# Kernel tuning notes

Measured on AMD Instinct MI355X. Metric: run time of the kernel, lower is better.

Reference implementation:

```python
import jax, jax.numpy as jnp
import numpy as np

EPS = 1e-5
HEADS, DK, DV = 8, 32, 64
SCALE = DK ** -0.5

def _bn(x, gamma, beta, mean, var):
    # eval-mode BatchNorm1d over channel dim of [b, c, n]
    inv = gamma / jnp.sqrt(var + EPS)
    return (x - mean[None, :, None]) * inv[None, :, None] + beta[None, :, None]

def setup_inputs() -> dict:
    key = jax.random.key(0)
    ks = jax.random.split(key, 24)
    dim, n, dim_out = 256, 1024, 256
    idk, idv = DK * HEADS, DV * HEADS
    def bn_params(k, c):
        k1, k2, k3, k4 = jax.random.split(k, 4)
        return (jax.random.normal(k1, (c,)) * 0.1 + 1.0,   # gamma
                jax.random.normal(k2, (c,)) * 0.1,          # beta
                jax.random.normal(k3, (c,)) * 0.1,          # running mean
                jax.random.uniform(k4, (c,)) * 0.5 + 0.5)   # running var > 0
    q_g, q_b, q_m, q_v = bn_params(ks[1], idk)
    k_g, k_b, k_m, k_v = bn_params(ks[2], idk)
    v_g, v_b, v_m, v_v = bn_params(ks[3], idv)
    o_g, o_b, o_m, o_v = bn_params(ks[4], dim_out)
    return {
        'x': jax.random.normal(ks[0], (8, dim, n), dtype=jnp.float32),
        'Wq': jax.random.normal(ks[5], (idk, dim)) * (dim ** -0.5),
        'Wk': jax.random.normal(ks[6], (idk, dim)) * (dim ** -0.5),
        'Wv': jax.random.normal(ks[7], (idv, dim)) * (dim ** -0.5),
        'Wo': jax.random.normal(ks[8], (dim_out, idv)) * (idv ** -0.5),
        'bo': jax.random.normal(ks[9], (dim_out,)) * 0.02,
        'pos_emb': jax.random.normal(ks[10], (n, HEADS)) * 0.02,
        'q_gamma': q_g, 'q_beta': q_b, 'q_mean': q_m, 'q_var': q_v,
        'k_gamma': k_g, 'k_beta': k_b, 'k_mean': k_m, 'k_var': k_v,
        'v_gamma': v_g, 'v_beta': v_b, 'v_mean': v_m, 'v_var': v_v,
        'o_gamma': o_g, 'o_beta': o_b, 'o_mean': o_m, 'o_var': o_v,
    }

def reference(x, Wq, Wk, Wv, Wo, bo, pos_emb,
              q_gamma, q_beta, q_mean, q_var,
              k_gamma, k_beta, k_mean, k_var,
              v_gamma, v_beta, v_mean, v_var,
              o_gamma, o_beta, o_mean, o_var):
    b, _, n = x.shape
    # 1x1 conv == channel matmul, then BN
    q = _bn(jnp.einsum('bcn,oc->bon', x, Wq), q_gamma, q_beta, q_mean, q_var)
    k = _bn(jnp.einsum('bcn,oc->bon', x, Wk), k_gamma, k_beta, k_mean, k_var)
    v = _bn(jnp.einsum('bcn,oc->bon', x, Wv), v_gamma, v_beta, v_mean, v_var)
    # b (h d) n -> b h n d
    q = q.reshape(b, HEADS, DK, n).transpose(0, 1, 3, 2)
    k = k.reshape(b, HEADS, DK, n).transpose(0, 1, 3, 2)
    v = v.reshape(b, HEADS, DV, n).transpose(0, 1, 3, 2)
    dots = jnp.einsum('bhid,bhjd->bhij', q, k) * SCALE
    # relative-position bias: emb[|i-j|] -> [n, n, h] -> [1, h, n, n]
    rel = jnp.abs(jnp.arange(n)[:, None] - jnp.arange(n)[None, :])
    bias = pos_emb[rel].transpose(2, 0, 1)[None]
    dots = dots + bias / SCALE
    attn = jax.nn.softmax(dots, axis=-1)
    out = jnp.einsum('bhij,bhjd->bhid', attn, v)
    # b h n d -> b (h d) n
    out = out.transpose(0, 1, 3, 2).reshape(b, HEADS * DV, n)
    out = jax.nn.gelu(out, approximate=False)
    out = jnp.einsum('bcn,oc->bon', out, Wo) + bo[None, :, None]
    return _bn(out, o_gamma, o_beta, o_mean, o_var)
```

## Files before the change

### kernel.cpp

```cpp
#include <hip/hip_runtime.h>
#include <hip/hip_bf16.h>

#define HEADS 8
#define DK 32
#define DV 64
#define DIM 256
#define NCTX 1024
#define NB 8
#define IDK 256
#define IDV 512
#define SCALE 0.17677669529663687f
#define INV_SCALE 5.656854249492381f
#define LOG2E 1.4426950408889634f
#define BN_EPS 1e-5f
#define THR 11.5416f

typedef __bf16 bf16x8 __attribute__((ext_vector_type(8)));
typedef __bf16 bf16x4 __attribute__((ext_vector_type(4)));
typedef float f32x4 __attribute__((ext_vector_type(4)));
typedef float f32x16 __attribute__((ext_vector_type(16)));

static __device__ __forceinline__ unsigned short bfbits(float v) {
  __bf16 b = (__bf16)v;
  return __builtin_bit_cast(unsigned short, b);
}

__global__ __launch_bounds__(256) void k_prep_trans(
    const float* __restrict__ x,
    const float* __restrict__ Wq, const float* __restrict__ Wk,
    const float* __restrict__ Wv, const float* __restrict__ Wo,
    const float* __restrict__ bo, const float* __restrict__ pe,
    const float* __restrict__ qg, const float* __restrict__ qb,
    const float* __restrict__ qm, const float* __restrict__ qv,
    const float* __restrict__ kg, const float* __restrict__ kb,
    const float* __restrict__ km, const float* __restrict__ kv,
    const float* __restrict__ vg, const float* __restrict__ vb,
    const float* __restrict__ vm, const float* __restrict__ vv,
    const float* __restrict__ og, const float* __restrict__ ob,
    const float* __restrict__ om, const float* __restrict__ ov,
    __bf16* __restrict__ xT, __bf16* __restrict__ WB, float* __restrict__ BB,
    uint2* __restrict__ Tq4g) {
  int bid = blockIdx.x;
  if (bid < 1605) {
    int idx = bid * 256 + threadIdx.x;
    if (idx < 65536) {
      int o = idx >> 8;
      WB[idx] = (__bf16)(Wq[idx] * (qg[o] * rsqrtf(qv[o] + BN_EPS) * SCALE * LOG2E));
    } else if (idx < 131072) {
      int i = idx - 65536, o = i >> 8;
      WB[idx] = (__bf16)(Wk[i] * (kg[o] * rsqrtf(kv[o] + BN_EPS)));
    } else if (idx < 262144) {
      int i = idx - 131072, o = i >> 8;
      WB[idx] = (__bf16)(Wv[i] * (vg[o] * rsqrtf(vv[o] + BN_EPS)));
    } else if (idx < 393216) {
      int i = idx - 262144, o = i >> 9;
      WB[idx] = (__bf16)(Wo[i] * (og[o] * rsqrtf(ov[o] + BN_EPS)));
    } else if (idx < 394496) {
      int i = idx - 393216;
      if (i < 256) {
        float sc = qg[i] * rsqrtf(qv[i] + BN_EPS);
        BB[i] = (qb[i] - qm[i] * sc) * SCALE * LOG2E;
      } else if (i < 512) {
        int o = i - 256;
        float sc = kg[o] * rsqrtf(kv[o] + BN_EPS);
        BB[i] = kb[o] - km[o] * sc;
      } else if (i < 1024) {
        int o = i - 512;
        float sc = vg[o] * rsqrtf(vv[o] + BN_EPS);
        BB[i] = vb[o] - vm[o] * sc;
      } else {
        int o = i - 1024;
        float sc = og[o] * rsqrtf(ov[o] + BN_EPS);
        BB[i] = (bo[o] - om[o]) * sc + ob[o];
      }
    } else {
      int i = idx - 394496;
      int h = i >> 11, t = i & 2047;
      unsigned short us[4];
#pragma unroll
      for (int rr = 0; rr < 4; ++rr) {
        int d = t - rr - 1023; d = d < 0 ? -d : d; d = d > 1023 ? 1023 : d;
        us[rr] = bfbits(pe[(size_t)d * HEADS + h] * INV_SCALE * LOG2E);
      }
      uint2 e;
      e.x = (unsigned)us[0] | ((unsigned)us[1] << 16);
      e.y = (unsigned)us[2] | ((unsigned)us[3] << 16);
      Tq4g[((size_t)h << 11) + t] = e;
    }
  } else {
    __shared__ float t[64][65];
    int tb = bid - 1605;
    int b = tb >> 6, c0 = ((tb >> 4) & 3) * 64, n0 = (tb & 15) * 64;
    int col = threadIdx.x & 63, rb = threadIdx.x >> 6;
    const float* xp = x + ((size_t)b * DIM + c0) * NCTX + n0;
#pragma unroll
    for (int r = 0; r < 16; ++r) {
      int row = rb + 4 * r;
      t[row][col] = xp[(size_t)row * NCTX + col];
    }
    __syncthreads();
    __bf16* op = xT + ((size_t)b * NCTX + n0) * DIM + c0;
#pragma unroll
    for (int r = 0; r < 16; ++r) {
      int i = rb + 4 * r;
      op[(size_t)i * DIM + col] = (__bf16)t[col][i];
    }
  }
}

__global__ __launch_bounds__(256, 2) void k_gemm_qkv(
    const __bf16* __restrict__ Xsrc, const __bf16* __restrict__ Wsrc,
    const float* __restrict__ Bias, __bf16* __restrict__ Qws,
    __bf16* __restrict__ Kws, __bf16* __restrict__ Vws) {
  int bx = blockIdx.x, by = blockIdx.y;
  int mode = by < 2 ? 0 : (by < 4 ? 1 : 2);
  int tid = threadIdx.x, wave = tid >> 6, lane = tid & 63;
  int wm = wave >> 1, wn = wave & 1;
  int l16 = lane & 15, g = (lane >> 4) & 3, g4 = g * 4;
  int R0 = bx * 128;

  __shared__ __align__(16) char XTl[16384];
  __shared__ __align__(16) char WTl[16384];

  int sr = tid >> 1, sh = tid & 1;
  const __bf16* xg = Xsrc + (size_t)(R0 + sr) * DIM + sh * 32;
  const __bf16* wg = Wsrc + (size_t)(by * 128 + sr) * DIM + sh * 32;
  int wbase = sr * 128;
  int gsw[4];
#pragma unroll
  for (int q = 0; q < 4; ++q) gsw[q] = ((sh * 4 + q) ^ (sr & 7)) * 16;

  bf16x8 sx[4], sw[4];
#pragma unroll
  for (int q = 0; q < 4; ++q) {
    sx[q] = *reinterpret_cast<const bf16x8*>(xg + q * 8);
    sw[q] = *reinterpret_cast<const bf16x8*>(wg + q * 8);
  }

  f32x4 acc[4][4] = {};
  const char* Abase = (mode <= 1) ? WTl : XTl;
  const char* Bbase = (mode <= 1) ? XTl : WTl;

  for (int st = 0; st < 4; ++st) {
    __syncthreads();
#pragma unroll
    for (int q = 0; q < 4; ++q) {
      *reinterpret_cast<bf16x8*>(XTl + wbase + gsw[q]) = sx[q];
      *reinterpret_cast<bf16x8*>(WTl + wbase + gsw[q]) = sw[q];
    }
    __syncthreads();
    if (st + 1 < 4) {
      const __bf16* xn = xg + (st + 1) * 64;
      const __bf16* wn_ = wg + (st + 1) * 64;
#pragma unroll
      for (int q = 0; q < 4; ++q) {
        sx[q] = *reinterpret_cast<const bf16x8*>(xn + q * 8);
        sw[q] = *reinterpret_cast<const bf16x8*>(wn_ + q * 8);
      }
    }
#pragma unroll
    for (int kc = 0; kc < 2; ++kc) {
      bf16x8 af[4], bf[4];
#pragma unroll
      for (int t = 0; t < 4; ++t) {
        int ra = wm * 64 + t * 16 + l16;
        af[t] = *reinterpret_cast<const bf16x8*>(
            Abase + ra * 128 + (((kc * 4 + g) ^ (ra & 7)) * 16));
        int rb = wn * 64 + t * 16 + l16;
        bf[t] = *reinterpret_cast<const bf16x8*>(
            Bbase + rb * 128 + (((kc * 4 + g) ^ (rb & 7)) * 16));
      }
      __builtin_amdgcn_s_setprio(1);
#pragma unroll
      for (int mt = 0; mt < 4; ++mt)
#pragma unroll
        for (int nt = 0; nt < 4; ++nt)
          acc[mt][nt] = __builtin_amdgcn_mfma_f32_16x16x32_bf16(
              af[mt], bf[nt], acc[mt][nt], 0, 0, 0);
      __builtin_amdgcn_s_setprio(0);
    }
  }

  if (mode <= 1) {
    __bf16* OWS = (mode == 0) ? Qws : Kws;
    const float* bb = Bias + (mode == 0 ? 0 : 256);
    int oq0 = by * 128 - (mode == 1 ? 256 : 0) + wm * 64;
#pragma unroll
    for (int mt = 0; mt < 4; ++mt) {
      int oq = oq0 + mt * 16 + g4;
      float4 b4 = *reinterpret_cast<const float4*>(&bb[oq]);
      int h = oq >> 5, d0 = oq & 31;
#pragma unroll
      for (int nt = 0; nt < 4; ++nt) {
        int i = R0 + wn * 64 + nt * 16 + l16;
        int b = i >> 10, n = i & 1023;
        bf16x4 pk;
        pk[0] = (__bf16)(acc[mt][nt][0] + b4.x);
        pk[1] = (__bf16)(acc[mt][nt][1] + b4.y);
        pk[2] = (__bf16)(acc[mt][nt][2] + b4.z);
        pk[3] = (__bf16)(acc[mt][nt][3] + b4.w);
        *reinterpret_cast<bf16x4*>(
            &OWS[(((size_t)b * HEADS + h) * NCTX + n) * DK + d0]) = pk;
      }
    }
  } else {
#pragma unroll
    for (int nt = 0; nt < 4; ++nt) {
      int vo = (by - 4) * 128 + wn * 64 + nt * 16 + l16;
      float bia = Bias[512 + vo];
#pragma unroll
      for (int mt = 0; mt < 4; ++mt) {
        int i0 = R0 + wm * 64 + mt * 16 + g4;
        int b = i0 >> 10, n = i0 & 1023;
        bf16x4 pk;
#pragma unroll
        for (int rr = 0; rr < 4; ++rr) pk[rr] = (__bf16)(acc[mt][nt][rr] + bia);
        *reinterpret_cast<bf16x4*>(&Vws[((size_t)b * IDV + vo) * NCTX + n]) = pk;
      }
    }
  }
}

__global__ __launch_bounds__(256, 4) void k_gemm_out(
    const __bf16* __restrict__ G, const __bf16* __restrict__ WoB,
    const float* __restrict__ bo2, float* __restrict__ out) {
  int bx = blockIdx.x, by = blockIdx.y;
  int tid = threadIdx.x, wave = tid >> 6, lane = tid & 63;
  int wm = wave >> 1, wn = wave & 1;
  int l16 = lane & 15, g = (lane >> 4) & 3, g4 = g * 4;
  int R0 = bx * 64;

  __shared__ __align__(16) char XTl[8192];
  __shared__ __align__(16) char WTl[8192];

  int sr = tid >> 2, sq = tid & 3;
  const __bf16* xg = G + (size_t)(R0 + sr) * IDV + sq * 16;
  const __bf16* wg = WoB + (size_t)(by * 64 + sr) * IDV + sq * 16;
  int sbase = sr * 128;
  int gswq[2];
#pragma unroll
  for (int q = 0; q < 2; ++q) gswq[q] = ((sq * 2 + q) ^ (sr & 7)) * 16;

  bf16x8 sx[2], sw[2];
#pragma unroll
  for (int q = 0; q < 2; ++q) {
    sx[q] = *reinterpret_cast<const bf16x8*>(xg + q * 8);
    sw[q] = *reinterpret_cast<const bf16x8*>(wg + q * 8);
  }

  f32x4 acc[2][2] = {};

  for (int st = 0; st < 8; ++st) {
    __syncthreads();
#pragma unroll
    for (int q = 0; q < 2; ++q) {
      *reinterpret_cast<bf16x8*>(XTl + sbase + gswq[q]) = sx[q];
      *reinterpret_cast<bf16x8*>(WTl + sbase + gswq[q]) = sw[q];
    }
    __syncthreads();
    if (st + 1 < 8) {
      const __bf16* xn = xg + (st + 1) * 64;
      const __bf16* wn_ = wg + (st + 1) * 64;
#pragma unroll
      for (int q = 0; q < 2; ++q) {
        sx[q] = *reinterpret_cast<const bf16x8*>(xn + q * 8);
        sw[q] = *reinterpret_cast<const bf16x8*>(wn_ + q * 8);
      }
    }
#pragma unroll
    for (int kc = 0; kc < 2; ++kc) {
      bf16x8 af[2], bf[2];
#pragma unroll
      for (int t = 0; t < 2; ++t) {
        int ra = wm * 32 + t * 16 + l16;
        af[t] = *reinterpret_cast<const bf16x8*>(
            XTl + ra * 128 + (((kc * 4 + g) ^ (ra & 7)) * 16));
        int rb = wn * 32 + t * 16 + l16;
        bf[t] = *reinterpret_cast<const bf16x8*>(
            WTl + rb * 128 + (((kc * 4 + g) ^ (rb & 7)) * 16));
      }
      __builtin_amdgcn_s_setprio(1);
#pragma unroll
      for (int mt = 0; mt < 2; ++mt)
#pragma unroll
        for (int nt = 0; nt < 2; ++nt)
          acc[mt][nt] = __builtin_amdgcn_mfma_f32_16x16x32_bf16(
              af[mt], bf[nt], acc[mt][nt], 0, 0, 0);
      __builtin_amdgcn_s_setprio(0);
    }
  }
#pragma unroll
  for (int nt = 0; nt < 2; ++nt) {
    int o = by * 64 + wn * 32 + nt * 16 + l16;
    float bia = bo2[o];
#pragma unroll
    for (int mt = 0; mt < 2; ++mt) {
      int i0 = R0 + wm * 32 + mt * 16 + g4;
      int b = i0 >> 10, n = i0 & 1023;
      float4 st;
      st.x = acc[mt][nt][0] + bia;
      st.y = acc[mt][nt][1] + bia;
      st.z = acc[mt][nt][2] + bia;
      st.w = acc[mt][nt][3] + bia;
      *reinterpret_cast<float4*>(&out[((size_t)b * DIM + o) * NCTX + n]) = st;
    }
  }
}

__global__ __launch_bounds__(256, 4) void k_attn(
    const __bf16* __restrict__ Qws, const __bf16* __restrict__ Kws,
    const __bf16* __restrict__ Vws, const uint2* __restrict__ Tq4g,
    __bf16* __restrict__ G) {
  int flat = blockIdx.x;
  int swz = (flat & 7) * 64 + (flat >> 3);
  int iblk = swz & 7, bh = swz >> 3;
  int b = bh >> 3, h = bh & 7;
  int tid = threadIdx.x, wave = tid >> 6, lane = tid & 63;
  int l31 = lane & 31, hi = lane >> 5;

  __shared__ __align__(16) __bf16 Klds[2][64][40];
  __shared__ __align__(16) __bf16 Vlds[2][64 * 64];
  __shared__ __align__(16) uint2 TqL[1152];

  int i0b = iblk * 128;
  {
    const uint4* tg4 = reinterpret_cast<const uint4*>(Tq4g + ((size_t)h << 11) + i0b);
    uint4* tl4 = reinterpret_cast<uint4*>(TqL);
    for (int c = tid; c < 576; c += 256) tl4[c] = tg4[c];
  }

  int i0w = i0b + wave * 32;
  int irow = i0w + l31;
  const __bf16* qbase = Qws + (size_t)bh * NCTX * DK;
  const __bf16* kbase = Kws + (size_t)bh * NCTX * DK;
  const __bf16* vbase = Vws + ((size_t)b * IDV + h * DV) * NCTX;
  bf16x8 qf0 = *reinterpret_cast<const bf16x8*>(qbase + (size_t)irow * DK + 8 * hi);
  bf16x8 qf1 = *reinterpret_cast<const bf16x8*>(qbase + (size_t)irow * DK + 16 + 8 * hi);

  int r_ = tid >> 2, sk = tid & 3;
  const __bf16* kgp = kbase + (size_t)r_ * DK + 8 * sk;
  const __bf16* vgp = vbase + (size_t)r_ * NCTX + 8 * sk;
  int ko = r_ * 40 + 8 * sk;
  int vo0 = r_ * 64 + 8 * (sk ^ (r_ & 7));
  int vo1 = r_ * 64 + 8 * ((sk + 4) ^ (r_ & 7));

  bf16x8 rk = *reinterpret_cast<const bf16x8*>(kgp);
  bf16x8 rv0 = *reinterpret_cast<const bf16x8*>(vgp);
  bf16x8 rv1 = *reinterpret_cast<const bf16x8*>(vgp + 32);
  *reinterpret_cast<bf16x8*>(&Klds[0][0][0] + ko) = rk;
  *reinterpret_cast<bf16x8*>(&Vlds[0][0] + vo0) = rv0;
  *reinterpret_cast<bf16x8*>(&Vlds[0][0] + vo1) = rv1;

  f32x16 acc0 = {}, acc1 = {};
  float m = -1e30f, s = 0.0f;
  int kxb = wave * 32 + l31 + 1023 - 4 * hi;
  const bf16x4* Tqp = reinterpret_cast<const bf16x4*>(TqL);

  __syncthreads();

  for (int it = 0; it < 16; ++it) {
    int cur = it & 1, nxt = cur ^ 1;
    int j0 = it * 64;
    int jn = (j0 + 64) & (NCTX - 1);
    rk = *reinterpret_cast<const bf16x8*>(kgp + (size_t)jn * DK);
    rv0 = *reinterpret_cast<const bf16x8*>(vgp + jn);
    rv1 = *reinterpret_cast<const bf16x8*>(vgp + jn + 32);

    float sv[32];
#pragma unroll
    for (int jg = 0; jg < 2; ++jg) {
      bf16x8 kf0 = *reinterpret_cast<const bf16x8*>(&Klds[cur][32 * jg + l31][8 * hi]);
      bf16x8 kf1 = *reinterpret_cast<const bf16x8*>(&Klds[cur][32 * jg + l31][16 + 8 * hi]);
      f32x16 S = {};
      __builtin_amdgcn_s_setprio(1);
      S = __builtin_amdgcn_mfma_f32_32x32x16_bf16(kf0, qf0, S, 0, 0, 0);
      S = __builtin_amdgcn_mfma_f32_32x32x16_bf16(kf1, qf1, S, 0, 0, 0);
      __builtin_amdgcn_s_setprio(0);
      int kb_ = kxb - j0 - 32 * jg;
#pragma unroll
      for (int q = 0; q < 4; ++q) {
        bf16x4 q4 = Tqp[kb_ - 8 * q];
#pragma unroll
        for (int rr = 0; rr < 4; ++rr)
          sv[jg * 16 + q * 4 + rr] = S[q * 4 + rr] + (float)q4[rr];
      }
    }
    float pmax = sv[0];
#pragma unroll
    for (int k = 1; k < 32; ++k) pmax = fmaxf(pmax, sv[k]);
    if (__any(pmax > m + THR)) {
      float mx = fmaxf(pmax, __shfl_xor(pmax, 32));
      float mnew = fmaxf(m, mx);
      float corr = __builtin_amdgcn_exp2f(m - mnew);
      s *= corr; m = mnew;
#pragma unroll
      for (int r = 0; r < 16; ++r) {
        float cv = __shfl(corr, (r & 3) + 8 * (r >> 2) + 4 * hi);
        acc0[r] *= cv; acc1[r] *= cv;
      }
    }
#pragma unroll
    for (int k = 0; k < 32; ++k) sv[k] = __builtin_amdgcn_exp2f(sv[k] - m);
    float ps = 0.0f;
#pragma unroll
    for (int k = 0; k < 32; ++k) ps += sv[k];
    s += ps;
#pragma unroll
    for (int jg = 0; jg < 2; ++jg) {
#pragma unroll
      for (int u = 0; u < 2; ++u) {
        int base = jg * 16 + 8 * u;
        unsigned we0, we1, wo0, wo1;
        asm("v_cvt_pk_bf16_f32 %0, %1, %2" : "=v"(we0) : "v"(sv[base + 0]), "v"(sv[base + 1]));
        asm("v_cvt_pk_bf16_f32 %0, %1, %2" : "=v"(we1) : "v"(sv[base + 2]), "v"(sv[base + 3]));
        asm("v_cvt_pk_bf16_f32 %0, %1, %2" : "=v"(wo0) : "v"(sv[base + 4]), "v"(sv[base + 5]));
        asm("v_cvt_pk_bf16_f32 %0, %1, %2" : "=v"(wo1) : "v"(sv[base + 6]), "v"(sv[base + 7]));
        asm volatile("v_permlane32_swap_b32 %0, %1" : "+v"(we0), "+v"(wo0));
        asm volatile("v_permlane32_swap_b32 %0, %1" : "+v"(we1), "+v"(wo1));
        uint4 pw = {we0, we1, wo0, wo1};
        bf16x8 pfrag = *reinterpret_cast<bf16x8*>(&pw);
        int sl = 2 * (jg * 2 + u) + hi;
        bf16x8 vf0 = *reinterpret_cast<const bf16x8*>(
            &Vlds[cur][0] + l31 * 64 + 8 * (sl ^ (l31 & 7)));
        bf16x8 vf1 = *reinterpret_cast<const bf16x8*>(
            &Vlds[cur][0] + (32 + l31) * 64 + 8 * (sl ^ (l31 & 7)));
        __builtin_amdgcn_s_setprio(1);
        acc0 = __builtin_amdgcn_mfma_f32_32x32x16_bf16(pfrag, vf0, acc0, 0, 0, 0);
        acc1 = __builtin_amdgcn_mfma_f32_32x32x16_bf16(pfrag, vf1, acc1, 0, 0, 0);
        __builtin_amdgcn_s_setprio(0);
      }
    }
    *reinterpret_cast<bf16x8*>(&Klds[nxt][0][0] + ko) = rk;
    *reinterpret_cast<bf16x8*>(&Vlds[nxt][0] + vo0) = rv0;
    *reinterpret_cast<bf16x8*>(&Vlds[nxt][0] + vo1) = rv1;
    __syncthreads();
  }
  float srow = s + __shfl_xor(s, 32);
  float inv = 1.0f / srow;
  __bf16* gbase = G + (size_t)b * NCTX * IDV + h * DV + l31;
#pragma unroll
  for (int r = 0; r < 16; ++r) {
    int il = (r & 3) + 8 * (r >> 2) + 4 * hi;
    float iv = __shfl(inv, il);
    float v0 = acc0[r] * iv, v1 = acc1[r] * iv;
    float g0 = 0.5f * v0 * (1.0f + erff(v0 * 0.70710678118654752f));
    float g1 = 0.5f * v1 * (1.0f + erff(v1 * 0.70710678118654752f));
    gbase[(size_t)(i0w + il) * IDV] = (__bf16)g0;
    gbase[(size_t)(i0w + il) * IDV + 32] = (__bf16)g1;
  }
}

extern "C" void kernel_launch(void* const* d_in, const int* in_sizes, int n_in,
                              void* d_out, int out_size, void* d_ws, size_t ws_size,
                              hipStream_t stream) {
  const float* x  = (const float*)d_in[0];
  const float* Wq = (const float*)d_in[1];
  const float* Wk = (const float*)d_in[2];
  const float* Wv = (const float*)d_in[3];
  const float* Wo = (const float*)d_in[4];
  const float* bo = (const float*)d_in[5];
  const float* pe = (const float*)d_in[6];
  const float* qg = (const float*)d_in[7];
  const float* qb = (const float*)d_in[8];
  const float* qm = (const float*)d_in[9];
  const float* qv = (const float*)d_in[10];
  const float* kg = (const float*)d_in[11];
  const float* kb = (const float*)d_in[12];
  const float* km = (const float*)d_in[13];
  const float* kv = (const float*)d_in[14];
  const float* vg = (const float*)d_in[15];
  const float* vb = (const float*)d_in[16];
  const float* vm = (const float*)d_in[17];
  const float* vv = (const float*)d_in[18];
  const float* og = (const float*)d_in[19];
  const float* ob = (const float*)d_in[20];
  const float* om = (const float*)d_in[21];
  const float* ov = (const float*)d_in[22];

  char* ws = (char*)d_ws;
  __bf16* xT = (__bf16*)(ws);
  __bf16* Q  = (__bf16*)(ws + (4ull << 20));
  __bf16* K  = (__bf16*)(ws + (8ull << 20));
  __bf16* V  = (__bf16*)(ws + (12ull << 20));
  __bf16* G  = (__bf16*)(ws + (20ull << 20));
  __bf16* WB = (__bf16*)(ws + (28ull << 20));
  float*  BB = (float*)(ws + (28ull << 20) + (768ull << 10));
  uint2*  Tq = (uint2*)(ws + (29ull << 20));
  float* out = (float*)d_out;

  k_prep_trans<<<dim3(2117), 256, 0, stream>>>(
      x, Wq, Wk, Wv, Wo, bo, pe, qg, qb, qm, qv, kg, kb, km, kv,
      vg, vb, vm, vv, og, ob, om, ov, xT, WB, BB, Tq);
  k_gemm_qkv<<<dim3(64, 8), 256, 0, stream>>>(xT, WB, BB, Q, K, V);
  k_attn<<<dim3(512), 256, 0, stream>>>(Q, K, V, Tq, G);
  k_gemm_out<<<dim3(128, 4), 256, 0, stream>>>(G, WB + 262144, BB + 1024, out);
}
```

Baseline: 56.78 us.

## Deepen attention K/V prefetch to two tiles ahead with register ping-pong

The attention loop is unrolled by two so K/V global loads are issued two tiles ahead into alternating register sets (A/B), while the LDS double buffer stays. This gives global loads more time in flight before their LDS store. It costs more registers, so the launch bound drops from 4 to 3 blocks per SM, which reduces occupancy.

```diff
diff --git a/kernel.cpp b/kernel.cpp
--- a/kernel.cpp
+++ b/kernel.cpp
@@ -307,7 +307,7 @@
   }
 }
 
-__global__ __launch_bounds__(256, 4) void k_attn(
+__global__ __launch_bounds__(256, 3) void k_attn(
     const __bf16* __restrict__ Qws, const __bf16* __restrict__ Kws,
     const __bf16* __restrict__ Vws, const uint2* __restrict__ Tq4g,
     __bf16* __restrict__ G) {
@@ -344,97 +344,127 @@
   int vo0 = r_ * 64 + 8 * (sk ^ (r_ & 7));
   int vo1 = r_ * 64 + 8 * ((sk + 4) ^ (r_ & 7));
 
-  bf16x8 rk = *reinterpret_cast<const bf16x8*>(kgp);
-  bf16x8 rv0 = *reinterpret_cast<const bf16x8*>(vgp);
-  bf16x8 rv1 = *reinterpret_cast<const bf16x8*>(vgp + 32);
-  *reinterpret_cast<bf16x8*>(&Klds[0][0][0] + ko) = rk;
-  *reinterpret_cast<bf16x8*>(&Vlds[0][0] + vo0) = rv0;
-  *reinterpret_cast<bf16x8*>(&Vlds[0][0] + vo1) = rv1;
-
   f32x16 acc0 = {}, acc1 = {};
   float m = -1e30f, s = 0.0f;
   int kxb = wave * 32 + l31 + 1023 - 4 * hi;
   const bf16x4* Tqp = reinterpret_cast<const bf16x4*>(TqL);
 
+  {
+    bf16x8 t0k = *reinterpret_cast<const bf16x8*>(kgp);
+    bf16x8 t0v0 = *reinterpret_cast<const bf16x8*>(vgp);
+    bf16x8 t0v1 = *reinterpret_cast<const bf16x8*>(vgp + 32);
+    *reinterpret_cast<bf16x8*>(&Klds[0][0][0] + ko) = t0k;
+    *reinterpret_cast<bf16x8*>(&Vlds[0][0] + vo0) = t0v0;
+    *reinterpret_cast<bf16x8*>(&Vlds[0][0] + vo1) = t0v1;
+  }
+  bf16x8 kA = *reinterpret_cast<const bf16x8*>(kgp + (size_t)64 * DK);
+  bf16x8 v0A = *reinterpret_cast<const bf16x8*>(vgp + 64);
+  bf16x8 v1A = *reinterpret_cast<const bf16x8*>(vgp + 96);
+  bf16x8 kB, v0B, v1B;
+
   __syncthreads();
 
-  for (int it = 0; it < 16; ++it) {
-    int cur = it & 1, nxt = cur ^ 1;
-    int j0 = it * 64;
-    int jn = (j0 + 64) & (NCTX - 1);
-    rk = *reinterpret_cast<const bf16x8*>(kgp + (size_t)jn * DK);
-    rv0 = *reinterpret_cast<const bf16x8*>(vgp + jn);
-    rv1 = *reinterpret_cast<const bf16x8*>(vgp + jn + 32);
-
-    float sv[32];
-#pragma unroll
-    for (int jg = 0; jg < 2; ++jg) {
-      bf16x8 kf0 = *reinterpret_cast<const bf16x8*>(&Klds[cur][32 * jg + l31][8 * hi]);
-      bf16x8 kf1 = *reinterpret_cast<const bf16x8*>(&Klds[cur][32 * jg + l31][16 + 8 * hi]);
-      f32x16 S = {};
-      __builtin_amdgcn_s_setprio(1);
-      S = __builtin_amdgcn_mfma_f32_32x32x16_bf16(kf0, qf0, S, 0, 0, 0);
-      S = __builtin_amdgcn_mfma_f32_32x32x16_bf16(kf1, qf1, S, 0, 0, 0);
-      __builtin_amdgcn_s_setprio(0);
-      int kb_ = kxb - j0 - 32 * jg;
-#pragma unroll
-      for (int q = 0; q < 4; ++q) {
-        bf16x4 q4 = Tqp[kb_ - 8 * q];
-#pragma unroll
-        for (int rr = 0; rr < 4; ++rr)
-          sv[jg * 16 + q * 4 + rr] = S[q * 4 + rr] + (float)q4[rr];
-      }
-    }
-    float pmax = sv[0];
-#pragma unroll
-    for (int k = 1; k < 32; ++k) pmax = fmaxf(pmax, sv[k]);
-    if (__any(pmax > m + THR)) {
-      float mx = fmaxf(pmax, __shfl_xor(pmax, 32));
-      float mnew = fmaxf(m, mx);
-      float corr = __builtin_amdgcn_exp2f(m - mnew);
-      s *= corr; m = mnew;
-#pragma unroll
-      for (int r = 0; r < 16; ++r) {
-        float cv = __shfl(corr, (r & 3) + 8 * (r >> 2) + 4 * hi);
-        acc0[r] *= cv; acc1[r] *= cv;
-      }
-    }
-#pragma unroll
-    for (int k = 0; k < 32; ++k) sv[k] = __builtin_amdgcn_exp2f(sv[k] - m);
-    float ps = 0.0f;
-#pragma unroll
-    for (int k = 0; k < 32; ++k) ps += sv[k];
-    s += ps;
-#pragma unroll
-    for (int jg = 0; jg < 2; ++jg) {
-#pragma unroll
-      for (int u = 0; u < 2; ++u) {
-        int base = jg * 16 + 8 * u;
-        unsigned we0, we1, wo0, wo1;
-        asm("v_cvt_pk_bf16_f32 %0, %1, %2" : "=v"(we0) : "v"(sv[base + 0]), "v"(sv[base + 1]));
-        asm("v_cvt_pk_bf16_f32 %0, %1, %2" : "=v"(we1) : "v"(sv[base + 2]), "v"(sv[base + 3]));
-        asm("v_cvt_pk_bf16_f32 %0, %1, %2" : "=v"(wo0) : "v"(sv[base + 4]), "v"(sv[base + 5]));
-        asm("v_cvt_pk_bf16_f32 %0, %1, %2" : "=v"(wo1) : "v"(sv[base + 6]), "v"(sv[base + 7]));
-        asm volatile("v_permlane32_swap_b32 %0, %1" : "+v"(we0), "+v"(wo0));
-        asm volatile("v_permlane32_swap_b32 %0, %1" : "+v"(we1), "+v"(wo1));
-        uint4 pw = {we0, we1, wo0, wo1};
-        bf16x8 pfrag = *reinterpret_cast<bf16x8*>(&pw);
-        int sl = 2 * (jg * 2 + u) + hi;
-        bf16x8 vf0 = *reinterpret_cast<const bf16x8*>(
-            &Vlds[cur][0] + l31 * 64 + 8 * (sl ^ (l31 & 7)));
-        bf16x8 vf1 = *reinterpret_cast<const bf16x8*>(
-            &Vlds[cur][0] + (32 + l31) * 64 + 8 * (sl ^ (l31 & 7)));
-        __builtin_amdgcn_s_setprio(1);
-        acc0 = __builtin_amdgcn_mfma_f32_32x32x16_bf16(pfrag, vf0, acc0, 0, 0, 0);
-        acc1 = __builtin_amdgcn_mfma_f32_32x32x16_bf16(pfrag, vf1, acc1, 0, 0, 0);
-        __builtin_amdgcn_s_setprio(0);
-      }
-    }
-    *reinterpret_cast<bf16x8*>(&Klds[nxt][0][0] + ko) = rk;
-    *reinterpret_cast<bf16x8*>(&Vlds[nxt][0] + vo0) = rv0;
-    *reinterpret_cast<bf16x8*>(&Vlds[nxt][0] + vo1) = rv1;
-    __syncthreads();
-  }
+#define ATTN_STEP(CUR, J0)                                                        \
+  {                                                                               \
+    float sv[32];                                                                 \
+    _Pragma("unroll")                                                             \
+    for (int jg = 0; jg < 2; ++jg) {                                              \
+      bf16x8 kf0 = *reinterpret_cast<const bf16x8*>(                              \
+          &Klds[CUR][32 * jg + l31][8 * hi]);                                     \
+      bf16x8 kf1 = *reinterpret_cast<const bf16x8*>(                              \
+          &Klds[CUR][32 * jg + l31][16 + 8 * hi]);                                \
+      f32x16 S = {};                                                              \
+      __builtin_amdgcn_s_setprio(1);                                              \
+      S = __builtin_amdgcn_mfma_f32_32x32x16_bf16(kf0, qf0, S, 0, 0, 0);          \
+      S = __builtin_amdgcn_mfma_f32_32x32x16_bf16(kf1, qf1, S, 0, 0, 0);          \
+      __builtin_amdgcn_s_setprio(0);                                              \
+      int kb_ = kxb - (J0) - 32 * jg;                                             \
+      _Pragma("unroll")                                                           \
+      for (int q = 0; q < 4; ++q) {                                               \
+        bf16x4 q4 = Tqp[kb_ - 8 * q];                                             \
+        _Pragma("unroll")                                                         \
+        for (int rr = 0; rr < 4; ++rr)                                            \
+          sv[jg * 16 + q * 4 + rr] = S[q * 4 + rr] + (float)q4[rr];               \
+      }                                                                           \
+    }                                                                             \
+    float pmax = sv[0];                                                           \
+    _Pragma("unroll")                                                             \
+    for (int k = 1; k < 32; ++k) pmax = fmaxf(pmax, sv[k]);                       \
+    if (__any(pmax > m + THR)) {                                                  \
+      float mx = fmaxf(pmax, __shfl_xor(pmax, 32));                               \
+      float mnew = fmaxf(m, mx);                                                  \
+      float corr = __builtin_amdgcn_exp2f(m - mnew);                              \
+      s *= corr; m = mnew;                                                        \
+      _Pragma("unroll")                                                           \
+      for (int r = 0; r < 16; ++r) {                                              \
+        float cv = __shfl(corr, (r & 3) + 8 * (r >> 2) + 4 * hi);                 \
+        acc0[r] *= cv; acc1[r] *= cv;                                             \
+      }                                                                           \
+    }                                                                             \
+    _Pragma("unroll")                                                             \
+    for (int k = 0; k < 32; ++k) sv[k] = __builtin_amdgcn_exp2f(sv[k] - m);       \
+    float ps = 0.0f;                                                              \
+    _Pragma("unroll")                                                             \
+    for (int k = 0; k < 32; ++k) ps += sv[k];                                     \
+    s += ps;                                                                      \
+    _Pragma("unroll")                                                             \
+    for (int jg = 0; jg < 2; ++jg) {                                              \
+      _Pragma("unroll")                                                           \
+      for (int u = 0; u < 2; ++u) {                                               \
+        int base = jg * 16 + 8 * u;                                               \
+        unsigned we0, we1, wo0, wo1;                                              \
+        asm("v_cvt_pk_bf16_f32 %0, %1, %2"                                        \
+            : "=v"(we0) : "v"(sv[base + 0]), "v"(sv[base + 1]));                  \
+        asm("v_cvt_pk_bf16_f32 %0, %1, %2"                                        \
+            : "=v"(we1) : "v"(sv[base + 2]), "v"(sv[base + 3]));                  \
+        asm("v_cvt_pk_bf16_f32 %0, %1, %2"                                        \
+            : "=v"(wo0) : "v"(sv[base + 4]), "v"(sv[base + 5]));                  \
+        asm("v_cvt_pk_bf16_f32 %0, %1, %2"                                        \
+            : "=v"(wo1) : "v"(sv[base + 6]), "v"(sv[base + 7]));                  \
+        asm volatile("v_permlane32_swap_b32 %0, %1" : "+v"(we0), "+v"(wo0));      \
+        asm volatile("v_permlane32_swap_b32 %0, %1" : "+v"(we1), "+v"(wo1));      \
+        uint4 pw = {we0, we1, wo0, wo1};                                          \
+        bf16x8 pfrag = *reinterpret_cast<bf16x8*>(&pw);                           \
+        int sl = 2 * (jg * 2 + u) + hi;                                           \
+        bf16x8 vf0 = *reinterpret_cast<const bf16x8*>(                            \
+            &Vlds[CUR][0] + l31 * 64 + 8 * (sl ^ (l31 & 7)));                     \
+        bf16x8 vf1 = *reinterpret_cast<const bf16x8*>(                            \
+            &Vlds[CUR][0] + (32 + l31) * 64 + 8 * (sl ^ (l31 & 7)));              \
+        __builtin_amdgcn_s_setprio(1);                                            \
+        acc0 = __builtin_amdgcn_mfma_f32_32x32x16_bf16(pfrag, vf0, acc0, 0,0,0);  \
+        acc1 = __builtin_amdgcn_mfma_f32_32x32x16_bf16(pfrag, vf1, acc1, 0,0,0);  \
+        __builtin_amdgcn_s_setprio(0);                                            \
+      }                                                                           \
+    }                                                                             \
+  }
+
+  for (int it2 = 0; it2 < 8; ++it2) {
+    int t = it2 * 2;
+    {
+      int jn = ((t + 2) * 64) & (NCTX - 1);
+      kB = *reinterpret_cast<const bf16x8*>(kgp + (size_t)jn * DK);
+      v0B = *reinterpret_cast<const bf16x8*>(vgp + jn);
+      v1B = *reinterpret_cast<const bf16x8*>(vgp + jn + 32);
+      ATTN_STEP(0, t * 64);
+      *reinterpret_cast<bf16x8*>(&Klds[1][0][0] + ko) = kA;
+      *reinterpret_cast<bf16x8*>(&Vlds[1][0] + vo0) = v0A;
+      *reinterpret_cast<bf16x8*>(&Vlds[1][0] + vo1) = v1A;
+      __syncthreads();
+    }
+    {
+      int jn = ((t + 3) * 64) & (NCTX - 1);
+      kA = *reinterpret_cast<const bf16x8*>(kgp + (size_t)jn * DK);
+      v0A = *reinterpret_cast<const bf16x8*>(vgp + jn);
+      v1A = *reinterpret_cast<const bf16x8*>(vgp + jn + 32);
+      ATTN_STEP(1, (t + 1) * 64);
+      *reinterpret_cast<bf16x8*>(&Klds[0][0][0] + ko) = kB;
+      *reinterpret_cast<bf16x8*>(&Vlds[0][0] + vo0) = v0B;
+      *reinterpret_cast<bf16x8*>(&Vlds[0][0] + vo1) = v1B;
+      __syncthreads();
+    }
+  }
+#undef ATTN_STEP
+
   float srow = s + __shfl_xor(s, 32);
   float inv = 1.0f / srow;
   __bf16* gbase = G + (size_t)b * NCTX * IDV + h * DV + l31;
```

Result: no change. 56.85 us (median of 2 runs) (+0.1%).
